# Kernel tuning notes

Measured on AMD Instinct MI355X. Metric: run time of the kernel, lower is better.

## Reference

```python
import jax, jax.numpy as jnp
import numpy as np

N_NODES = 50000
N_EDGES = 800000
D_IN = 128
D_HID = 128


def gcn_conv(x, W, b, src, dst, ew, n_nodes):
    """PyG GCNConv: add self-loops (weight 1), symmetric deg^-1/2 normalization,
    aggregate messages from src at dst, then h = Ahat x W + b."""
    # linear transform first (PyG applies lin before propagate)
    h = x @ W  # [N, D_out]
    loops = jnp.arange(n_nodes, dtype=src.dtype)
    s = jnp.concatenate([src, loops])
    d = jnp.concatenate([dst, loops])
    w = jnp.concatenate([ew, jnp.ones((n_nodes,), dtype=ew.dtype)])
    deg = jax.ops.segment_sum(w, d, num_segments=n_nodes)  # [N]
    dinv = jnp.where(deg > 0, jax.lax.rsqrt(deg), 0.0)
    norm = dinv[s] * w * dinv[d]  # [E+N]
    msg = norm[:, None] * h[s]  # [E+N, D_out]
    out = jax.ops.segment_sum(msg, d, num_segments=n_nodes)
    return out + b


def setup_inputs() -> dict:
    key = jax.random.key(0)
    k1, k2, k3, k4, k5 = jax.random.split(key, 5)
    x = jax.random.normal(k1, (N_NODES, D_IN), dtype=jnp.float32)
    edge_index = jax.random.randint(k2, (2, N_EDGES), 0, N_NODES, dtype=jnp.int64)
    edge_weight = jax.random.uniform(k3, (N_EDGES,), dtype=jnp.float32)
    # glorot-style init for GCN layer weights
    s1 = 1.0 / np.sqrt(D_IN)
    s2 = 1.0 / np.sqrt(D_HID)
    W1 = jax.random.uniform(k4, (D_IN, D_HID), minval=-s1, maxval=s1, dtype=jnp.float32)
    W2 = jax.random.uniform(k5, (D_HID, D_HID), minval=-s2, maxval=s2, dtype=jnp.float32)
    b1 = jnp.zeros((D_HID,), dtype=jnp.float32)
    b2 = jnp.zeros((D_HID,), dtype=jnp.float32)
    return {"x": x, "edge_index": edge_index, "edge_weight": edge_weight,
            "W1": W1, "b1": b1, "W2": W2, "b2": b2}


def reference(x, edge_index, edge_weight, W1, b1, W2, b2):
    n = x.shape[0]
    src, dst = edge_index[0], edge_index[1]
    x1 = jax.nn.relu(gcn_conv(x, W1, b1, src, dst, edge_weight, n))
    x2 = jax.nn.relu(gcn_conv(x1, W2, b2, src, dst, edge_weight, n))
    return jnp.concatenate([x1[:, :, None], x2[:, :, None]], axis=2)  # [N, D_HID, 2]
```

## Files before the change

kernel.cpp:

```cpp
#include <hip/hip_runtime.h>

#define NN 50000
#define NE 800000
#define D 128
#define SCAN_CH 1024
#define SCAN_NB ((NN + SCAN_CH - 1) / SCAN_CH)

typedef __attribute__((ext_vector_type(8))) short short8;
typedef __attribute__((ext_vector_type(4))) float f32x4;
typedef unsigned short ushort;
typedef unsigned int uint;
typedef unsigned long long u64;

__device__ inline ushort f2b(float x) {
    uint u = __float_as_uint(x);
    return (ushort)((u + 0x7fffu + ((u >> 16) & 1u)) >> 16);
}
__device__ inline float blo(uint u) { return __uint_as_float(u << 16); }
__device__ inline float bhi(uint u) { return __uint_as_float(u & 0xffff0000u); }


__global__ __launch_bounds__(256) void k_init_wt(u64* __restrict__ pc,
                                                 const float* __restrict__ W1,
                                                 const float* __restrict__ W2,
                                                 ushort* __restrict__ wtb1,
                                                 ushort* __restrict__ wtb2, int n) {
    int g = blockIdx.x * 256 + threadIdx.x;
    if (g < n) pc[g] = 0ull;
    if (g < 2 * D * D) {
        const float* W = (g < D * D) ? W1 : W2;
        ushort* wt = (g < D * D) ? wtb1 : wtb2;
        int idx = (g < D * D) ? g : g - D * D;
        int k = idx >> 7, c = idx & 127;
        wt[c * D + k] = f2b(W[idx]);
    }
}


__global__ __launch_bounds__(256) void k_deg_cnt(const int* __restrict__ dst,
                                                 const float* __restrict__ ew,
                                                 u64* __restrict__ pc,
                                                 int* __restrict__ erank, int e4) {
    int i = blockIdx.x * 256 + threadIdx.x;
    if (i >= e4) return;
    int4 d4 = *(const int4*)&dst[i * 4];
    float4 w4 = *(const float4*)&ew[i * 4];
    int4 r4;
    {
        uint fx = (uint)(w4.x * 16777216.0f + 0.5f);
        r4.x = (int)(atomicAdd(&pc[d4.x], (1ull << 32) | (u64)fx) >> 32);
    }
    {
        uint fx = (uint)(w4.y * 16777216.0f + 0.5f);
        r4.y = (int)(atomicAdd(&pc[d4.y], (1ull << 32) | (u64)fx) >> 32);
    }
    {
        uint fx = (uint)(w4.z * 16777216.0f + 0.5f);
        r4.z = (int)(atomicAdd(&pc[d4.z], (1ull << 32) | (u64)fx) >> 32);
    }
    {
        uint fx = (uint)(w4.w * 16777216.0f + 0.5f);
        r4.w = (int)(atomicAdd(&pc[d4.w], (1ull << 32) | (u64)fx) >> 32);
    }
    *(int4*)&erank[i * 4] = r4;
}


__global__ __launch_bounds__(256) void k_scan_part(const u64* __restrict__ pc,
                                                   int* __restrict__ blockSums,
                                                   float* __restrict__ rsd, int n) {
    __shared__ int s[256];
    const int tid = threadIdx.x;
    const int base = blockIdx.x * SCAN_CH + tid * 4;
    int c0 = 0, c1 = 0, c2 = 0, c3 = 0;
    const float sc = 1.0f / 16777216.0f;
    if (base + 3 < n) {
        u64 p0 = pc[base + 0], p1 = pc[base + 1], p2 = pc[base + 2], p3 = pc[base + 3];
        c0 = (int)(p0 >> 32); c1 = (int)(p1 >> 32);
        c2 = (int)(p2 >> 32); c3 = (int)(p3 >> 32);
        float4 dv;
        dv.x = rsqrtf(1.0f + (float)(uint)p0 * sc);
        dv.y = rsqrtf(1.0f + (float)(uint)p1 * sc);
        dv.z = rsqrtf(1.0f + (float)(uint)p2 * sc);
        dv.w = rsqrtf(1.0f + (float)(uint)p3 * sc);
        *(float4*)&rsd[base] = dv;
    } else {
        for (int j = 0; j < 4; ++j) {
            if (base + j < n) {
                u64 p = pc[base + j];
                int cj = (int)(p >> 32);
                if (j == 0) c0 = cj; else if (j == 1) c1 = cj; else if (j == 2) c2 = cj; else c3 = cj;
                rsd[base + j] = rsqrtf(1.0f + (float)(uint)p * sc);
            }
        }
    }
    s[tid] = c0 + c1 + c2 + c3;
    __syncthreads();
    for (int off = 1; off < 256; off <<= 1) {
        int v = s[tid];
        int add = (tid >= off) ? s[tid - off] : 0;
        __syncthreads();
        s[tid] = v + add;
        __syncthreads();
    }
    if (tid == 255) blockSums[blockIdx.x] = s[255];
}


__global__ __launch_bounds__(256) void k_scan_add(const u64* __restrict__ pc,
                                                  const int* __restrict__ blockSums,
                                                  int* __restrict__ rowptr, int n, int e) {
    __shared__ int s[256];
    __shared__ int s_boff;
    const int tid = threadIdx.x;
    if (tid < 64) {
        int v = (tid < SCAN_NB) ? blockSums[tid] : 0;
        int inc = v;
#pragma unroll
        for (int off = 1; off < 64; off <<= 1) {
            int u = __shfl_up(inc, off);
            if (tid >= off) inc += u;
        }
        if (tid == blockIdx.x) s_boff = inc - v;
    }
    const int base = blockIdx.x * SCAN_CH + tid * 4;
    int c0 = 0, c1 = 0, c2 = 0, c3 = 0;
    if (base + 3 < n) {
        c0 = (int)(pc[base + 0] >> 32); c1 = (int)(pc[base + 1] >> 32);
        c2 = (int)(pc[base + 2] >> 32); c3 = (int)(pc[base + 3] >> 32);
    } else {
        if (base + 0 < n) c0 = (int)(pc[base + 0] >> 32);
        if (base + 1 < n) c1 = (int)(pc[base + 1] >> 32);
        if (base + 2 < n) c2 = (int)(pc[base + 2] >> 32);
    }
    int tsum = c0 + c1 + c2 + c3;
    s[tid] = tsum;
    __syncthreads();
    for (int off = 1; off < 256; off <<= 1) {
        int v = s[tid];
        int add = (tid >= off) ? s[tid - off] : 0;
        __syncthreads();
        s[tid] = v + add;
        __syncthreads();
    }
    int p = s_boff + s[tid] - tsum;
    int p0 = p, p1 = p + c0, p2 = p + c0 + c1, p3 = p + c0 + c1 + c2;
    if (base + 3 < n) {
        *(int4*)&rowptr[base] = make_int4(p0, p1, p2, p3);
    } else {
        if (base + 0 < n) rowptr[base + 0] = p0;
        if (base + 1 < n) rowptr[base + 1] = p1;
        if (base + 2 < n) rowptr[base + 2] = p2;
    }
    if (blockIdx.x == 0 && tid == 0) rowptr[n] = e;
}


__global__ __launch_bounds__(256) void k_scatter(const int* __restrict__ src,
                                                 const int* __restrict__ dst,
                                                 const float* __restrict__ ew,
                                                 const int* __restrict__ rowptr,
                                                 const int* __restrict__ erank,
                                                 int2* __restrict__ edges, int e) {
    int i = blockIdx.x * 256 + threadIdx.x;
    if (i >= e) return;
    int d = dst[i];
    int pos = rowptr[d] + erank[i];
    int2 ev;
    ev.x = src[i];
    ev.y = __float_as_int(ew[i]);
    edges[pos] = ev;
}


__global__ __launch_bounds__(256) void k_gemm(const float* __restrict__ A,
                                              const ushort* __restrict__ wtb,
                                              const float* __restrict__ rsd,
                                              ushort* __restrict__ h, int n) {
    __shared__ ushort bounce[4][16][136];
    const int w = threadIdx.x >> 6, l = threadIdx.x & 63;
    const int r = l & 15, hg = l >> 4;
    const int node = blockIdx.x * 64 + w * 16 + r;
    const bool valid = node < n;
    const float* arow = A + (size_t)(valid ? node : 0) * D;

    short8 afr[4];
#pragma unroll
    for (int kk = 0; kk < 4; ++kk) {
        float4 p = *(const float4*)(arow + kk * 32 + hg * 8);
        float4 q = *(const float4*)(arow + kk * 32 + hg * 8 + 4);
        short8 t;
        t[0] = (short)f2b(p.x); t[1] = (short)f2b(p.y);
        t[2] = (short)f2b(p.z); t[3] = (short)f2b(p.w);
        t[4] = (short)f2b(q.x); t[5] = (short)f2b(q.y);
        t[6] = (short)f2b(q.z); t[7] = (short)f2b(q.w);
        afr[kk] = t;
    }

    float rs[4];
#pragma unroll
    for (int g = 0; g < 4; ++g) {
        int nd = blockIdx.x * 64 + w * 16 + hg * 4 + g;
        rs[g] = (nd < n) ? rsd[nd] : 1.0f;
    }

#pragma unroll
    for (int ct = 0; ct < 8; ++ct) {
        f32x4 acc = {0.f, 0.f, 0.f, 0.f};
#pragma unroll
        for (int kk = 0; kk < 4; ++kk) {
            short8 b = *(const short8*)(wtb + (size_t)(ct * 16 + r) * D + kk * 32 + hg * 8);
            acc = __builtin_amdgcn_mfma_f32_16x16x32_bf16(afr[kk], b, acc, 0, 0, 0);
        }
#pragma unroll
        for (int g = 0; g < 4; ++g)
            bounce[w][hg * 4 + g][ct * 16 + r] = f2b(acc[g] * rs[g]);
    }
    __syncthreads();

#pragma unroll
    for (int it = 0; it < 4; ++it) {
        int cid = it * 64 + l;
        int nl = cid >> 4;
        int ch = cid & 15;
        int onode = blockIdx.x * 64 + w * 16 + nl;
        if (onode < n) {
            int4 vv = *(const int4*)&bounce[w][nl][ch * 8];
            *(int4*)(h + (size_t)onode * D + ch * 8) = vv;
        }
    }
}


#define AGG_BODY                                                               \
    float rv = rsd[v];                                                         \
    uint us = *(const uint*)(hb + (size_t)v * D + f);                          \
    float accx = blo(us);                                                      \
    float accy = bhi(us);                                                      \
    int beg = rowptr[v], end = rowptr[v + 1];                                  \
    for (int base = beg; base < end; base += 64) {                             \
        int idx = base + lane;                                                 \
        int2 ev = (idx < end) ? edges[idx] : make_int2(v, 0);                  \
        int mm = min(64, end - base);                                          \
        for (int sb = 0; sb < 4; ++sb) {                                       \
            if (sb * 16 >= mm) break;                                          \
            uint u[16];                                                        \
            float ws[16];                                                      \
            _Pragma("unroll")                                                  \
            for (int j = 0; j < 16; ++j) {                                     \
                int s = __builtin_amdgcn_readlane(ev.x, sb * 16 + j);          \
                ws[j] = __uint_as_float((uint)__builtin_amdgcn_readlane(ev.y, sb * 16 + j)); \
                u[j] = *(const uint*)(hb + (size_t)s * D + f);                 \
            }                                                                  \
            _Pragma("unroll")                                                  \
            for (int j = 0; j < 16; ++j) {                                     \
                accx += ws[j] * blo(u[j]);                                     \
                accy += ws[j] * bhi(u[j]);                                     \
            }                                                                  \
        }                                                                      \
    }

__global__ __launch_bounds__(256) void k_agg1(const int* __restrict__ rowptr,
                                              const int2* __restrict__ edges,
                                              const float* __restrict__ rsd,
                                              const ushort* __restrict__ hb,
                                              const float* __restrict__ b,
                                              float* __restrict__ x1, int n) {
    int v = (blockIdx.x * 256 + threadIdx.x) >> 6;
    if (v >= n) return;
    int lane = threadIdx.x & 63;
    int f = lane * 2;
    AGG_BODY
    float2 o;
    o.x = fmaxf(rv * accx + b[f + 0], 0.0f);
    o.y = fmaxf(rv * accy + b[f + 1], 0.0f);
    *(float2*)&x1[(size_t)v * D + f] = o;
}

__global__ __launch_bounds__(256) void k_agg2(const int* __restrict__ rowptr,
                                              const int2* __restrict__ edges,
                                              const float* __restrict__ rsd,
                                              const ushort* __restrict__ hb,
                                              const float* __restrict__ x1,
                                              const float* __restrict__ b,
                                              float* __restrict__ out, int n) {
    int v = (blockIdx.x * 256 + threadIdx.x) >> 6;
    if (v >= n) return;
    int lane = threadIdx.x & 63;
    int f = lane * 2;
    AGG_BODY
    float2 xv = *(const float2*)&x1[(size_t)v * D + f];
    float4 o;
    o.x = xv.x;
    o.y = fmaxf(rv * accx + b[f + 0], 0.0f);
    o.z = xv.y;
    o.w = fmaxf(rv * accy + b[f + 1], 0.0f);
    *(float4*)&out[((size_t)v * D + f) * 2] = o;
}

extern "C" void kernel_launch(void* const* d_in, const int* in_sizes, int n_in,
                              void* d_out, int out_size, void* d_ws, size_t ws_size,
                              hipStream_t stream) {
    const float* x  = (const float*)d_in[0];
    const int*   ei = (const int*)d_in[1];
    const float* ew = (const float*)d_in[2];
    const float* W1 = (const float*)d_in[3];
    const float* b1 = (const float*)d_in[4];
    const float* W2 = (const float*)d_in[5];
    const float* b2 = (const float*)d_in[6];
    float* out = (float*)d_out;

    const int* src = ei;
    const int* dst = ei + NE;

    char* w = (char*)d_ws;
    auto take = [&](size_t bytes) {
        char* p = w;
        w += (bytes + 255) & ~(size_t)255;
        return p;
    };
    u64*    pc        = (u64*)take((size_t)NN * 8);
    float*  rsd       = (float*)take((size_t)NN * 4);
    int*    rowptr    = (int*)take((size_t)(NN + 1) * 4);
    int*    blockSums = (int*)take((size_t)SCAN_NB * 4);
    int*    erank     = (int*)take((size_t)NE * 4);
    int2*   edges     = (int2*)take((size_t)NE * 8);
    ushort* wtb1      = (ushort*)take((size_t)D * D * 2);
    ushort* wtb2      = (ushort*)take((size_t)D * D * 2);
    ushort* hb        = (ushort*)take((size_t)NN * D * 2);
    float*  x1        = (float*)take((size_t)NN * D * 4);

    const int nBlkN   = (NN + 255) / 256;
    const int nBlkE   = (NE + 255) / 256;
    const int nBlkE4  = (NE / 4 + 255) / 256;
    const int nBlkG   = (NN + 63) / 64;
    const int nBlkAgg = (NN * 64 + 255) / 256;

    k_init_wt<<<nBlkN, 256, 0, stream>>>(pc, W1, W2, wtb1, wtb2, NN);
    k_deg_cnt<<<nBlkE4, 256, 0, stream>>>(dst, ew, pc, erank, NE / 4);
    k_scan_part<<<SCAN_NB, 256, 0, stream>>>(pc, blockSums, rsd, NN);
    k_scan_add<<<SCAN_NB, 256, 0, stream>>>(pc, blockSums, rowptr, NN, NE);
    k_scatter<<<nBlkE, 256, 0, stream>>>(src, dst, ew, rowptr, erank, edges, NE);

    k_gemm<<<nBlkG, 256, 0, stream>>>(x, wtb1, rsd, hb, NN);
    k_agg1<<<nBlkAgg, 256, 0, stream>>>(rowptr, edges, rsd, hb, b1, x1, NN);

    k_gemm<<<nBlkG, 256, 0, stream>>>(x1, wtb2, rsd, hb, NN);
    k_agg2<<<nBlkAgg, 256, 0, stream>>>(rowptr, edges, rsd, hb, x1, b2, out, NN);
}
```

Before: 257.1 us.

## Fuse all GCN stages into one cooperative persistent kernel with grid syncs

Replaces the nine separate launches (init, degree count, two scan passes, scatter, two GEMMs, two aggregations) with a single cooperative kernel whose grid-stride loops are separated by grid.sync barriers. It also keeps the layer-1 activations in bf16 instead of fp32, and writes the final output with nontemporal stores. The intent is to remove per-launch gaps and to cut memory traffic for the intermediate activations. In exchange it adds grid-wide barrier costs and caps the grid at a fixed number of resident blocks, which may lower latency hiding in the gather-heavy aggregation phases. The x1 half of the output is now rounded to bf16.

```diff
diff --git a/kernel.cpp b/kernel.cpp
--- a/kernel.cpp
+++ b/kernel.cpp
@@ -1,10 +1,14 @@
 #include <hip/hip_runtime.h>
+#include <hip/hip_cooperative_groups.h>
+
+namespace cg = cooperative_groups;
 
 #define NN 50000
 #define NE 800000
 #define D 128
 #define SCAN_CH 1024
 #define SCAN_NB ((NN + SCAN_CH - 1) / SCAN_CH)
+#define GMAX 1024
 
 typedef __attribute__((ext_vector_type(8))) short short8;
 typedef __attribute__((ext_vector_type(4))) float f32x4;
@@ -18,219 +22,6 @@
 }
 __device__ inline float blo(uint u) { return __uint_as_float(u << 16); }
 __device__ inline float bhi(uint u) { return __uint_as_float(u & 0xffff0000u); }
-
-
-__global__ __launch_bounds__(256) void k_init_wt(u64* __restrict__ pc,
-                                                 const float* __restrict__ W1,
-                                                 const float* __restrict__ W2,
-                                                 ushort* __restrict__ wtb1,
-                                                 ushort* __restrict__ wtb2, int n) {
-    int g = blockIdx.x * 256 + threadIdx.x;
-    if (g < n) pc[g] = 0ull;
-    if (g < 2 * D * D) {
-        const float* W = (g < D * D) ? W1 : W2;
-        ushort* wt = (g < D * D) ? wtb1 : wtb2;
-        int idx = (g < D * D) ? g : g - D * D;
-        int k = idx >> 7, c = idx & 127;
-        wt[c * D + k] = f2b(W[idx]);
-    }
-}
-
-
-__global__ __launch_bounds__(256) void k_deg_cnt(const int* __restrict__ dst,
-                                                 const float* __restrict__ ew,
-                                                 u64* __restrict__ pc,
-                                                 int* __restrict__ erank, int e4) {
-    int i = blockIdx.x * 256 + threadIdx.x;
-    if (i >= e4) return;
-    int4 d4 = *(const int4*)&dst[i * 4];
-    float4 w4 = *(const float4*)&ew[i * 4];
-    int4 r4;
-    {
-        uint fx = (uint)(w4.x * 16777216.0f + 0.5f);
-        r4.x = (int)(atomicAdd(&pc[d4.x], (1ull << 32) | (u64)fx) >> 32);
-    }
-    {
-        uint fx = (uint)(w4.y * 16777216.0f + 0.5f);
-        r4.y = (int)(atomicAdd(&pc[d4.y], (1ull << 32) | (u64)fx) >> 32);
-    }
-    {
-        uint fx = (uint)(w4.z * 16777216.0f + 0.5f);
-        r4.z = (int)(atomicAdd(&pc[d4.z], (1ull << 32) | (u64)fx) >> 32);
-    }
-    {
-        uint fx = (uint)(w4.w * 16777216.0f + 0.5f);
-        r4.w = (int)(atomicAdd(&pc[d4.w], (1ull << 32) | (u64)fx) >> 32);
-    }
-    *(int4*)&erank[i * 4] = r4;
-}
-
-
-__global__ __launch_bounds__(256) void k_scan_part(const u64* __restrict__ pc,
-                                                   int* __restrict__ blockSums,
-                                                   float* __restrict__ rsd, int n) {
-    __shared__ int s[256];
-    const int tid = threadIdx.x;
-    const int base = blockIdx.x * SCAN_CH + tid * 4;
-    int c0 = 0, c1 = 0, c2 = 0, c3 = 0;
-    const float sc = 1.0f / 16777216.0f;
-    if (base + 3 < n) {
-        u64 p0 = pc[base + 0], p1 = pc[base + 1], p2 = pc[base + 2], p3 = pc[base + 3];
-        c0 = (int)(p0 >> 32); c1 = (int)(p1 >> 32);
-        c2 = (int)(p2 >> 32); c3 = (int)(p3 >> 32);
-        float4 dv;
-        dv.x = rsqrtf(1.0f + (float)(uint)p0 * sc);
-        dv.y = rsqrtf(1.0f + (float)(uint)p1 * sc);
-        dv.z = rsqrtf(1.0f + (float)(uint)p2 * sc);
-        dv.w = rsqrtf(1.0f + (float)(uint)p3 * sc);
-        *(float4*)&rsd[base] = dv;
-    } else {
-        for (int j = 0; j < 4; ++j) {
-            if (base + j < n) {
-                u64 p = pc[base + j];
-                int cj = (int)(p >> 32);
-                if (j == 0) c0 = cj; else if (j == 1) c1 = cj; else if (j == 2) c2 = cj; else c3 = cj;
-                rsd[base + j] = rsqrtf(1.0f + (float)(uint)p * sc);
-            }
-        }
-    }
-    s[tid] = c0 + c1 + c2 + c3;
-    __syncthreads();
-    for (int off = 1; off < 256; off <<= 1) {
-        int v = s[tid];
-        int add = (tid >= off) ? s[tid - off] : 0;
-        __syncthreads();
-        s[tid] = v + add;
-        __syncthreads();
-    }
-    if (tid == 255) blockSums[blockIdx.x] = s[255];
-}
-
-
-__global__ __launch_bounds__(256) void k_scan_add(const u64* __restrict__ pc,
-                                                  const int* __restrict__ blockSums,
-                                                  int* __restrict__ rowptr, int n, int e) {
-    __shared__ int s[256];
-    __shared__ int s_boff;
-    const int tid = threadIdx.x;
-    if (tid < 64) {
-        int v = (tid < SCAN_NB) ? blockSums[tid] : 0;
-        int inc = v;
-#pragma unroll
-        for (int off = 1; off < 64; off <<= 1) {
-            int u = __shfl_up(inc, off);
-            if (tid >= off) inc += u;
-        }
-        if (tid == blockIdx.x) s_boff = inc - v;
-    }
-    const int base = blockIdx.x * SCAN_CH + tid * 4;
-    int c0 = 0, c1 = 0, c2 = 0, c3 = 0;
-    if (base + 3 < n) {
-        c0 = (int)(pc[base + 0] >> 32); c1 = (int)(pc[base + 1] >> 32);
-        c2 = (int)(pc[base + 2] >> 32); c3 = (int)(pc[base + 3] >> 32);
-    } else {
-        if (base + 0 < n) c0 = (int)(pc[base + 0] >> 32);
-        if (base + 1 < n) c1 = (int)(pc[base + 1] >> 32);
-        if (base + 2 < n) c2 = (int)(pc[base + 2] >> 32);
-    }
-    int tsum = c0 + c1 + c2 + c3;
-    s[tid] = tsum;
-    __syncthreads();
-    for (int off = 1; off < 256; off <<= 1) {
-        int v = s[tid];
-        int add = (tid >= off) ? s[tid - off] : 0;
-        __syncthreads();
-        s[tid] = v + add;
-        __syncthreads();
-    }
-    int p = s_boff + s[tid] - tsum;
-    int p0 = p, p1 = p + c0, p2 = p + c0 + c1, p3 = p + c0 + c1 + c2;
-    if (base + 3 < n) {
-        *(int4*)&rowptr[base] = make_int4(p0, p1, p2, p3);
-    } else {
-        if (base + 0 < n) rowptr[base + 0] = p0;
-        if (base + 1 < n) rowptr[base + 1] = p1;
-        if (base + 2 < n) rowptr[base + 2] = p2;
-    }
-    if (blockIdx.x == 0 && tid == 0) rowptr[n] = e;
-}
-
-
-__global__ __launch_bounds__(256) void k_scatter(const int* __restrict__ src,
-                                                 const int* __restrict__ dst,
-                                                 const float* __restrict__ ew,
-                                                 const int* __restrict__ rowptr,
-                                                 const int* __restrict__ erank,
-                                                 int2* __restrict__ edges, int e) {
-    int i = blockIdx.x * 256 + threadIdx.x;
-    if (i >= e) return;
-    int d = dst[i];
-    int pos = rowptr[d] + erank[i];
-    int2 ev;
-    ev.x = src[i];
-    ev.y = __float_as_int(ew[i]);
-    edges[pos] = ev;
-}
-
-
-__global__ __launch_bounds__(256) void k_gemm(const float* __restrict__ A,
-                                              const ushort* __restrict__ wtb,
-                                              const float* __restrict__ rsd,
-                                              ushort* __restrict__ h, int n) {
-    __shared__ ushort bounce[4][16][136];
-    const int w = threadIdx.x >> 6, l = threadIdx.x & 63;
-    const int r = l & 15, hg = l >> 4;
-    const int node = blockIdx.x * 64 + w * 16 + r;
-    const bool valid = node < n;
-    const float* arow = A + (size_t)(valid ? node : 0) * D;
-
-    short8 afr[4];
-#pragma unroll
-    for (int kk = 0; kk < 4; ++kk) {
-        float4 p = *(const float4*)(arow + kk * 32 + hg * 8);
-        float4 q = *(const float4*)(arow + kk * 32 + hg * 8 + 4);
-        short8 t;
-        t[0] = (short)f2b(p.x); t[1] = (short)f2b(p.y);
-        t[2] = (short)f2b(p.z); t[3] = (short)f2b(p.w);
-        t[4] = (short)f2b(q.x); t[5] = (short)f2b(q.y);
-        t[6] = (short)f2b(q.z); t[7] = (short)f2b(q.w);
-        afr[kk] = t;
-    }
-
-    float rs[4];
-#pragma unroll
-    for (int g = 0; g < 4; ++g) {
-        int nd = blockIdx.x * 64 + w * 16 + hg * 4 + g;
-        rs[g] = (nd < n) ? rsd[nd] : 1.0f;
-    }
-
-#pragma unroll
-    for (int ct = 0; ct < 8; ++ct) {
-        f32x4 acc = {0.f, 0.f, 0.f, 0.f};
-#pragma unroll
-        for (int kk = 0; kk < 4; ++kk) {
-            short8 b = *(const short8*)(wtb + (size_t)(ct * 16 + r) * D + kk * 32 + hg * 8);
-            acc = __builtin_amdgcn_mfma_f32_16x16x32_bf16(afr[kk], b, acc, 0, 0, 0);
-        }
-#pragma unroll
-        for (int g = 0; g < 4; ++g)
-            bounce[w][hg * 4 + g][ct * 16 + r] = f2b(acc[g] * rs[g]);
-    }
-    __syncthreads();
-
-#pragma unroll
-    for (int it = 0; it < 4; ++it) {
-        int cid = it * 64 + l;
-        int nl = cid >> 4;
-        int ch = cid & 15;
-        int onode = blockIdx.x * 64 + w * 16 + nl;
-        if (onode < n) {
-            int4 vv = *(const int4*)&bounce[w][nl][ch * 8];
-            *(int4*)(h + (size_t)onode * D + ch * 8) = vv;
-        }
-    }
-}
-
 
 #define AGG_BODY                                                               \
     float rv = rsd[v];                                                         \
@@ -260,42 +51,237 @@
         }                                                                      \
     }
 
-__global__ __launch_bounds__(256) void k_agg1(const int* __restrict__ rowptr,
-                                              const int2* __restrict__ edges,
-                                              const float* __restrict__ rsd,
-                                              const ushort* __restrict__ hb,
-                                              const float* __restrict__ b,
-                                              float* __restrict__ x1, int n) {
-    int v = (blockIdx.x * 256 + threadIdx.x) >> 6;
-    if (v >= n) return;
-    int lane = threadIdx.x & 63;
-    int f = lane * 2;
-    AGG_BODY
-    float2 o;
-    o.x = fmaxf(rv * accx + b[f + 0], 0.0f);
-    o.y = fmaxf(rv * accy + b[f + 1], 0.0f);
-    *(float2*)&x1[(size_t)v * D + f] = o;
-}
-
-__global__ __launch_bounds__(256) void k_agg2(const int* __restrict__ rowptr,
-                                              const int2* __restrict__ edges,
-                                              const float* __restrict__ rsd,
-                                              const ushort* __restrict__ hb,
-                                              const float* __restrict__ x1,
-                                              const float* __restrict__ b,
-                                              float* __restrict__ out, int n) {
-    int v = (blockIdx.x * 256 + threadIdx.x) >> 6;
-    if (v >= n) return;
-    int lane = threadIdx.x & 63;
-    int f = lane * 2;
-    AGG_BODY
-    float2 xv = *(const float2*)&x1[(size_t)v * D + f];
-    float4 o;
-    o.x = xv.x;
-    o.y = fmaxf(rv * accx + b[f + 0], 0.0f);
-    o.z = xv.y;
-    o.w = fmaxf(rv * accy + b[f + 1], 0.0f);
-    *(float4*)&out[((size_t)v * D + f) * 2] = o;
+__global__ __launch_bounds__(256, 4) void k_mega(
+    const float* __restrict__ x, const int* __restrict__ ei,
+    const float* __restrict__ ew, const float* __restrict__ W1,
+    const float* __restrict__ b1, const float* __restrict__ W2,
+    const float* __restrict__ b2, float* __restrict__ out,
+    u64* __restrict__ pc, float* __restrict__ rsd, int* __restrict__ rowptr,
+    int* __restrict__ blockSums, int* __restrict__ erank,
+    int2* __restrict__ edges, ushort* __restrict__ wtb1,
+    ushort* __restrict__ wtb2, ushort* __restrict__ hb,
+    ushort* __restrict__ x1b) {
+    cg::grid_group grid = cg::this_grid();
+    const int tid = threadIdx.x;
+    const int bid = blockIdx.x;
+    const int G = gridDim.x;
+    const int gthread = bid * 256 + tid;
+    const int NT = G * 256;
+    const int* src = ei;
+    const int* dstp = ei + NE;
+
+    __shared__ __align__(16) ushort bounce[4][16][136];
+    int* s = (int*)&bounce[0][0][0];
+    __shared__ int s_boff;
+
+    for (int i = gthread; i < NN; i += NT) pc[i] = 0ull;
+    for (int i = gthread; i < 2 * D * D; i += NT) {
+        const float* W = (i < D * D) ? W1 : W2;
+        ushort* wt = (i < D * D) ? wtb1 : wtb2;
+        int idx = (i < D * D) ? i : i - D * D;
+        int k = idx >> 7, c = idx & 127;
+        wt[c * D + k] = f2b(W[idx]);
+    }
+    grid.sync();
+
+    for (int i = gthread; i < NE / 4; i += NT) {
+        int4 d4 = *(const int4*)&dstp[i * 4];
+        float4 w4 = *(const float4*)&ew[i * 4];
+        int4 r4;
+        { uint fx = (uint)(w4.x * 16777216.0f + 0.5f);
+          r4.x = (int)(atomicAdd(&pc[d4.x], (1ull << 32) | (u64)fx) >> 32); }
+        { uint fx = (uint)(w4.y * 16777216.0f + 0.5f);
+          r4.y = (int)(atomicAdd(&pc[d4.y], (1ull << 32) | (u64)fx) >> 32); }
+        { uint fx = (uint)(w4.z * 16777216.0f + 0.5f);
+          r4.z = (int)(atomicAdd(&pc[d4.z], (1ull << 32) | (u64)fx) >> 32); }
+        { uint fx = (uint)(w4.w * 16777216.0f + 0.5f);
+          r4.w = (int)(atomicAdd(&pc[d4.w], (1ull << 32) | (u64)fx) >> 32); }
+        *(int4*)&erank[i * 4] = r4;
+    }
+    grid.sync();
+
+    if (bid < SCAN_NB) {
+        const int base = bid * SCAN_CH + tid * 4;
+        int c0 = 0, c1 = 0, c2 = 0, c3 = 0;
+        const float sc = 1.0f / 16777216.0f;
+        if (base + 3 < NN) {
+            u64 p0 = pc[base + 0], p1 = pc[base + 1], p2 = pc[base + 2], p3 = pc[base + 3];
+            c0 = (int)(p0 >> 32); c1 = (int)(p1 >> 32);
+            c2 = (int)(p2 >> 32); c3 = (int)(p3 >> 32);
+            float4 dv;
+            dv.x = rsqrtf(1.0f + (float)(uint)p0 * sc);
+            dv.y = rsqrtf(1.0f + (float)(uint)p1 * sc);
+            dv.z = rsqrtf(1.0f + (float)(uint)p2 * sc);
+            dv.w = rsqrtf(1.0f + (float)(uint)p3 * sc);
+            *(float4*)&rsd[base] = dv;
+        } else {
+            for (int j = 0; j < 4; ++j) {
+                if (base + j < NN) {
+                    u64 p = pc[base + j];
+                    int cj = (int)(p >> 32);
+                    if (j == 0) c0 = cj; else if (j == 1) c1 = cj; else if (j == 2) c2 = cj; else c3 = cj;
+                    rsd[base + j] = rsqrtf(1.0f + (float)(uint)p * sc);
+                }
+            }
+        }
+        s[tid] = c0 + c1 + c2 + c3;
+        __syncthreads();
+        for (int off = 1; off < 256; off <<= 1) {
+            int v = s[tid];
+            int add = (tid >= off) ? s[tid - off] : 0;
+            __syncthreads();
+            s[tid] = v + add;
+            __syncthreads();
+        }
+        if (tid == 255) blockSums[bid] = s[255];
+    }
+    grid.sync();
+
+    if (bid < SCAN_NB) {
+        if (tid < 64) {
+            int v = (tid < SCAN_NB) ? blockSums[tid] : 0;
+            int inc = v;
+#pragma unroll
+            for (int off = 1; off < 64; off <<= 1) {
+                int u = __shfl_up(inc, off);
+                if (tid >= off) inc += u;
+            }
+            if (tid == bid) s_boff = inc - v;
+        }
+        const int base = bid * SCAN_CH + tid * 4;
+        int c0 = 0, c1 = 0, c2 = 0, c3 = 0;
+        if (base + 3 < NN) {
+            c0 = (int)(pc[base + 0] >> 32); c1 = (int)(pc[base + 1] >> 32);
+            c2 = (int)(pc[base + 2] >> 32); c3 = (int)(pc[base + 3] >> 32);
+        } else {
+            if (base + 0 < NN) c0 = (int)(pc[base + 0] >> 32);
+            if (base + 1 < NN) c1 = (int)(pc[base + 1] >> 32);
+            if (base + 2 < NN) c2 = (int)(pc[base + 2] >> 32);
+        }
+        int tsum = c0 + c1 + c2 + c3;
+        s[tid] = tsum;
+        __syncthreads();
+        for (int off = 1; off < 256; off <<= 1) {
+            int v = s[tid];
+            int add = (tid >= off) ? s[tid - off] : 0;
+            __syncthreads();
+            s[tid] = v + add;
+            __syncthreads();
+        }
+        int p = s_boff + s[tid] - tsum;
+        int p0 = p, p1 = p + c0, p2 = p + c0 + c1, p3 = p + c0 + c1 + c2;
+        if (base + 3 < NN) {
+            *(int4*)&rowptr[base] = make_int4(p0, p1, p2, p3);
+        } else {
+            if (base + 0 < NN) rowptr[base + 0] = p0;
+            if (base + 1 < NN) rowptr[base + 1] = p1;
+            if (base + 2 < NN) rowptr[base + 2] = p2;
+        }
+        if (bid == 0 && tid == 0) rowptr[NN] = NE;
+    }
+    grid.sync();
+
+    for (int i = gthread; i < NE; i += NT) {
+        int d = dstp[i];
+        int pos = rowptr[d] + erank[i];
+        int2 ev;
+        ev.x = src[i];
+        ev.y = __float_as_int(ew[i]);
+        edges[pos] = ev;
+    }
+    grid.sync();
+
+    const int ntiles = (NN + 63) / 64;
+    const int w = tid >> 6, l = tid & 63;
+    const int r = l & 15, hg = l >> 4;
+    const int lane = l;
+    const int f = lane * 2;
+    const int wid0 = bid * 4 + w;
+    const int nw = G * 4;
+
+#pragma unroll 1
+    for (int layer = 0; layer < 2; ++layer) {
+        const ushort* wtb = layer ? wtb2 : wtb1;
+        const float* bias = layer ? b2 : b1;
+
+        for (int t = bid; t < ntiles; t += G) {
+            __syncthreads();
+            const int node = t * 64 + w * 16 + r;
+            const bool valid = node < NN;
+            short8 afr[4];
+            if (layer) {
+                const ushort* arow = x1b + (size_t)(valid ? node : 0) * D;
+#pragma unroll
+                for (int kk = 0; kk < 4; ++kk)
+                    afr[kk] = *(const short8*)(arow + kk * 32 + hg * 8);
+            } else {
+                const float* arow = x + (size_t)(valid ? node : 0) * D;
+#pragma unroll
+                for (int kk = 0; kk < 4; ++kk) {
+                    float4 p = *(const float4*)(arow + kk * 32 + hg * 8);
+                    float4 q = *(const float4*)(arow + kk * 32 + hg * 8 + 4);
+                    short8 tt;
+                    tt[0] = (short)f2b(p.x); tt[1] = (short)f2b(p.y);
+                    tt[2] = (short)f2b(p.z); tt[3] = (short)f2b(p.w);
+                    tt[4] = (short)f2b(q.x); tt[5] = (short)f2b(q.y);
+                    tt[6] = (short)f2b(q.z); tt[7] = (short)f2b(q.w);
+                    afr[kk] = tt;
+                }
+            }
+            float rs[4];
+#pragma unroll
+            for (int g = 0; g < 4; ++g) {
+                int nd = t * 64 + w * 16 + hg * 4 + g;
+                rs[g] = (nd < NN) ? rsd[nd] : 1.0f;
+            }
+#pragma unroll
+            for (int ct = 0; ct < 8; ++ct) {
+                f32x4 acc = {0.f, 0.f, 0.f, 0.f};
+#pragma unroll
+                for (int kk = 0; kk < 4; ++kk) {
+                    short8 bb = *(const short8*)(wtb + (size_t)(ct * 16 + r) * D + kk * 32 + hg * 8);
+                    acc = __builtin_amdgcn_mfma_f32_16x16x32_bf16(afr[kk], bb, acc, 0, 0, 0);
+                }
+#pragma unroll
+                for (int g = 0; g < 4; ++g)
+                    bounce[w][hg * 4 + g][ct * 16 + r] = f2b(acc[g] * rs[g]);
+            }
+            __syncthreads();
+#pragma unroll
+            for (int it = 0; it < 4; ++it) {
+                int cid = it * 64 + l;
+                int nl = cid >> 4;
+                int ch = cid & 15;
+                int onode = t * 64 + w * 16 + nl;
+                if (onode < NN) {
+                    int4 vv = *(const int4*)&bounce[w][nl][ch * 8];
+                    *(int4*)(hb + (size_t)onode * D + ch * 8) = vv;
+                }
+            }
+        }
+        grid.sync();
+
+        if (layer == 0) {
+            for (int v = wid0; v < NN; v += nw) {
+                AGG_BODY
+                uint ox = (uint)f2b(fmaxf(rv * accx + bias[f + 0], 0.0f));
+                uint oy = (uint)f2b(fmaxf(rv * accy + bias[f + 1], 0.0f));
+                *(uint*)&x1b[(size_t)v * D + f] = ox | (oy << 16);
+            }
+            grid.sync();
+        } else {
+            for (int v = wid0; v < NN; v += nw) {
+                AGG_BODY
+                uint xu = *(const uint*)&x1b[(size_t)v * D + f];
+                f32x4 o;
+                o[0] = blo(xu);
+                o[1] = fmaxf(rv * accx + bias[f + 0], 0.0f);
+                o[2] = bhi(xu);
+                o[3] = fmaxf(rv * accy + bias[f + 1], 0.0f);
+                __builtin_nontemporal_store(o, (f32x4*)&out[((size_t)v * D + f) * 2]);
+            }
+        }
+    }
 }
 
 extern "C" void kernel_launch(void* const* d_in, const int* in_sizes, int n_in,
@@ -309,9 +295,6 @@
     const float* W2 = (const float*)d_in[5];
     const float* b2 = (const float*)d_in[6];
     float* out = (float*)d_out;
-
-    const int* src = ei;
-    const int* dst = ei + NE;
 
     char* w = (char*)d_ws;
     auto take = [&](size_t bytes) {
@@ -328,23 +311,18 @@
     ushort* wtb1      = (ushort*)take((size_t)D * D * 2);
     ushort* wtb2      = (ushort*)take((size_t)D * D * 2);
     ushort* hb        = (ushort*)take((size_t)NN * D * 2);
-    float*  x1        = (float*)take((size_t)NN * D * 4);
-
-    const int nBlkN   = (NN + 255) / 256;
-    const int nBlkE   = (NE + 255) / 256;
-    const int nBlkE4  = (NE / 4 + 255) / 256;
-    const int nBlkG   = (NN + 63) / 64;
-    const int nBlkAgg = (NN * 64 + 255) / 256;
-
-    k_init_wt<<<nBlkN, 256, 0, stream>>>(pc, W1, W2, wtb1, wtb2, NN);
-    k_deg_cnt<<<nBlkE4, 256, 0, stream>>>(dst, ew, pc, erank, NE / 4);
-    k_scan_part<<<SCAN_NB, 256, 0, stream>>>(pc, blockSums, rsd, NN);
-    k_scan_add<<<SCAN_NB, 256, 0, stream>>>(pc, blockSums, rowptr, NN, NE);
-    k_scatter<<<nBlkE, 256, 0, stream>>>(src, dst, ew, rowptr, erank, edges, NE);
-
-    k_gemm<<<nBlkG, 256, 0, stream>>>(x, wtb1, rsd, hb, NN);
-    k_agg1<<<nBlkAgg, 256, 0, stream>>>(rowptr, edges, rsd, hb, b1, x1, NN);
-
-    k_gemm<<<nBlkG, 256, 0, stream>>>(x1, wtb2, rsd, hb, NN);
-    k_agg2<<<nBlkAgg, 256, 0, stream>>>(rowptr, edges, rsd, hb, x1, b2, out, NN);
+    ushort* x1b       = (ushort*)take((size_t)NN * D * 2);
+
+    int maxB = 0;
+    if (hipOccupancyMaxActiveBlocksPerMultiprocessor(&maxB, k_mega, 256, 0) != hipSuccess || maxB <= 0)
+        maxB = 2;
+    int G = maxB * 256;
+    if (G > GMAX) G = GMAX;
+
+    void* args[] = {(void*)&x,   (void*)&ei,   (void*)&ew,   (void*)&W1,
+                    (void*)&b1,  (void*)&W2,   (void*)&b2,   (void*)&out,
+                    (void*)&pc,  (void*)&rsd,  (void*)&rowptr, (void*)&blockSums,
+                    (void*)&erank, (void*)&edges, (void*)&wtb1, (void*)&wtb2,
+                    (void*)&hb,  (void*)&x1b};
+    (void)hipLaunchCooperativeKernel(k_mega, dim3(G), dim3(256), args, 0, stream);
 }
```

After: 770.8 us. +199.8%, slower.
